# Kernel optimization log

Measured on AMD Instinct MI355X. Metric: run time of the kernel, lower is better.

Reference implementation:

```python
import jax, jax.numpy as jnp
import numpy as np

VOCAB, HID, EMB = 32000, 512, 256
N, L = 256, 512


def setup_inputs() -> dict:
    key = jax.random.key(0)
    ks = jax.random.split(key, 6)
    X = jax.random.randint(ks[0], (N, L), 0, VOCAB)
    emb = jax.random.normal(ks[1], (VOCAB, EMB), dtype=jnp.float32) * 0.02
    # torch Linear: y = x @ W.T + b, W shape (out, in)
    Whh_w = jax.random.normal(ks[2], (HID, HID), dtype=jnp.float32) * (1.0 / np.sqrt(HID))
    Whh_b = jnp.zeros((HID,), dtype=jnp.float32)
    Wxh_w = jax.random.normal(ks[3], (HID, EMB), dtype=jnp.float32) * (1.0 / np.sqrt(EMB))
    Wxh_b = jnp.zeros((HID,), dtype=jnp.float32)
    return {"X": X, "emb": emb, "Whh_w": Whh_w, "Whh_b": Whh_b,
            "Wxh_w": Wxh_w, "Wxh_b": Wxh_b}


def reference(X, emb, Whh_w, Whh_b, Wxh_w, Wxh_b):
    # X: (N, L) int ids -> last hidden state (N, H)
    E = emb[X]                       # (N, L, E) embedding lookup
    # precompute input projection for all timesteps (one big GEMM)
    XP = jnp.einsum('nle,he->nlh', E, Wxh_w) + Wxh_b  # (N, L, H)
    h0 = jnp.zeros((X.shape[0], Whh_w.shape[0]), dtype=emb.dtype)

    def step(h, xp_t):
        # xp_t: (N, H) at time t
        h_new = jnp.tanh(h @ Whh_w.T + Whh_b + xp_t)
        return h_new, None

    h_last, _ = jax.lax.scan(step, h0, jnp.swapaxes(XP, 0, 1))  # scan over L
    return h_last
```

## Files before the change

kernel.cpp:

```cpp
#include <hip/hip_runtime.h>
#include <hip/hip_bf16.h>
#include <math.h>

#define N_B    256
#define L_SEQ  512
#define HID    512
#define EMB_D  256

#define NGROUPS 16
#define GWGS    8

#define ESW_SHORTS_PER_BLK 8192
#define ESW_BYTES  ((size_t)NGROUPS * L_SEQ * ESW_SHORTS_PER_BLK * 2)
#define EX_UINTS_PER_SLOT (16 * HID)
#define EX_BYTES   ((size_t)2 * NGROUPS * EX_UINTS_PER_SLOT * 4)

typedef short v8s __attribute__((ext_vector_type(8)));
typedef float v4f __attribute__((ext_vector_type(4)));

static __device__ __forceinline__ unsigned short bf_bits(__hip_bfloat16 h) {
    union { __hip_bfloat16 b; unsigned short u; } c; c.b = h; return c.u;
}
static __device__ __forceinline__ void split_hilo(float v, short& hi, short& lo) {
    const __hip_bfloat16 h = __float2bfloat16(v);
    hi = (short)bf_bits(h);
    lo = (short)bf_bits(__float2bfloat16(v - __bfloat162float(h)));
}
static __device__ __forceinline__ void cvt8_hilo(const float* __restrict__ p,
                                                 v8s& hi, v8s& lo) {
    #pragma unroll
    for (int i = 0; i < 8; ++i) { short h, l; split_hilo(p[i], h, l); hi[i] = h; lo[i] = l; }
}
static __device__ __forceinline__ void gl_lds16(const short* g, short* l) {
    __builtin_amdgcn_global_load_lds(
        (const __attribute__((address_space(1))) unsigned int*)g,
        (__attribute__((address_space(3))) unsigned int*)l, 16, 0, 0);
}
static __device__ __forceinline__ float tanh_fast(float x) {
    const float z = __expf(2.0f * x);
    return 1.0f - 2.0f / (z + 1.0f);
}

__global__ __launch_bounds__(256) void esw_build(
    const int* __restrict__ X, const float* __restrict__ emb,
    short* __restrict__ Esw)
{
    const int bid = blockIdx.x;
    const int g = bid >> 9, t = bid & 511;
    short* base = Esw + (size_t)bid * ESW_SHORTS_PER_BLK;
    #pragma unroll
    for (int h = 0; h < 2; ++h) {
        const int f    = threadIdx.x + h * 256;
        const int kk   = f >> 6, lane = f & 63;
        const int m    = lane & 15, qp = lane >> 4;
        const int idx  = X[(g * 16 + m) * L_SEQ + t];
        const float* src = emb + (size_t)idx * EMB_D + kk * 32 + qp * 8;
        v8s hi8, lo8;
        cvt8_hilo(src, hi8, lo8);
        short* d = base + (size_t)(kk * 64 + lane) * 8;
        *(v8s*)d          = hi8;
        *(v8s*)(d + 4096) = lo8;
    }
}

__global__ __launch_bounds__(256, 1) void rnn_scan5(
    const float* __restrict__ Whh,
    const float* __restrict__ Whh_b,
    const float* __restrict__ Wxh,
    const float* __restrict__ Wxh_b,
    const short* __restrict__ Esw,
    unsigned int* __restrict__ ex,
    float* __restrict__ out)
{
    const int bid  = blockIdx.x;
    const int g    = bid & 15;
    const int j    = bid >> 4;
    const int tid  = threadIdx.x;
    const int w    = tid >> 6;
    const int l    = tid & 63;
    const int lo16 = l & 15;
    const int q    = l >> 4;
    const int cbase = j * 64 + w * 16;
    const int nbase = g * 16;

    __shared__ short ldsbuf[49152];
    __shared__ unsigned int tp[4][256];
    short* lds_h = ldsbuf;
    short* lds_e = ldsbuf + 32768;

    v8s bhi[16], blo[16];
    {
        const float* wp = Whh + (long)(cbase + lo16) * HID + q * 8;
        #pragma unroll
        for (int kk = 0; kk < 16; ++kk) cvt8_hilo(wp + kk * 32, bhi[kk], blo[kk]);
    }
    v8s xhi[8], xlo[8];
    {
        const float* wp = Wxh + (long)(cbase + lo16) * EMB_D + q * 8;
        #pragma unroll
        for (int kk = 0; kk < 8; ++kk) cvt8_hilo(wp + kk * 32, xhi[kk], xlo[kk]);
    }
    const int hcol = cbase + lo16;
    const float bias = Whh_b[hcol] + Wxh_b[hcol];

    const int region = (2 * j + (w >> 1)) * 512 + (w & 1) * 256;

    unsigned int* ex0 = ex + (size_t)g * EX_UINTS_PER_SLOT;
    unsigned int* ex1 = ex + (size_t)(NGROUPS + g) * EX_UINTS_PER_SLOT;
    const short* esrc = Esw + (size_t)(g * 512) * ESW_SHORTS_PER_BLK;

    #pragma unroll
    for (int c = 0; c < 4; ++c)
        gl_lds16(esrc + (w * 4 + c) * 512 + l * 8, lds_e + (w * 4 + c) * 512);
    __syncthreads();

    for (int t = 0; t < L_SEQ; ++t) {
        const int P = t & 1;
        short* lh = lds_h + P * 16384;
        short* le = lds_e + P * 8192;
        unsigned int* exsrc = P ? ex1 : ex0;
        unsigned int* exdst = P ? ex0 : ex1;

        if (t + 1 < L_SEQ) {
            const short* eb = esrc + (size_t)(t + 1) * ESW_SHORTS_PER_BLK;
            short* leN = lds_e + (P ^ 1) * 8192;
            #pragma unroll
            for (int c = 0; c < 4; ++c)
                gl_lds16(eb + (w * 4 + c) * 512 + l * 8, leN + (w * 4 + c) * 512);
        }

        v4f acc0 = {0,0,0,0}, acc1 = {0,0,0,0}, acc2 = {0,0,0,0};
        #pragma unroll
        for (int kk = 0; kk < 8; ++kk) {
            v8s ah = *(const v8s*)(le + (kk * 64 + l) * 8);
            v8s al = *(const v8s*)(le + 4096 + (kk * 64 + l) * 8);
            acc0 = __builtin_amdgcn_mfma_f32_16x16x32_bf16(ah, xhi[kk], acc0, 0, 0, 0);
            acc1 = __builtin_amdgcn_mfma_f32_16x16x32_bf16(ah, xlo[kk], acc1, 0, 0, 0);
            acc2 = __builtin_amdgcn_mfma_f32_16x16x32_bf16(al, xhi[kk], acc2, 0, 0, 0);
        }

        unsigned long long hv64[16];
        {
            const unsigned long long* hs = (const unsigned long long*)exsrc;
            const unsigned long long tagmask = 0x0001000000010000ull;
            const unsigned long long want = ((t >> 1) & 1) ? tagmask : 0ull;
            for (;;) {
                #pragma unroll
                for (int s = 0; s < 16; ++s)
                    hv64[s] = __hip_atomic_load(hs + s * 256 + tid,
                                                __ATOMIC_RELAXED,
                                                __HIP_MEMORY_SCOPE_AGENT);
                unsigned long long bad = 0;
                #pragma unroll
                for (int s = 0; s < 16; ++s) bad |= (hv64[s] ^ want) & tagmask;
                if (__all(bad == 0)) break;
            }
        }

        {
            unsigned int* lh_hi = (unsigned int*)lh;
            unsigned int* lh_lo = lh_hi + 4096;
            #pragma unroll
            for (int s = 0; s < 16; ++s) {
                const int o = s * 256 + tid;
                const unsigned int w0 = (unsigned int)hv64[s];
                const unsigned int w1 = (unsigned int)(hv64[s] >> 32);
                lh_hi[o] = (w0 & 0xffffu) | (w1 << 16);
                lh_lo[o] = (w0 >> 16)     | (w1 & 0xffff0000u);
            }
        }
        __syncthreads();

        #pragma unroll
        for (int kk = 0; kk < 16; ++kk) {
            v8s ah = *(const v8s*)(lh + (kk * 64 + l) * 8);
            v8s al = *(const v8s*)(lh + 8192 + (kk * 64 + l) * 8);
            acc0 = __builtin_amdgcn_mfma_f32_16x16x32_bf16(ah, bhi[kk], acc0, 0, 0, 0);
            acc1 = __builtin_amdgcn_mfma_f32_16x16x32_bf16(ah, blo[kk], acc1, 0, 0, 0);
            acc2 = __builtin_amdgcn_mfma_f32_16x16x32_bf16(al, bhi[kk], acc2, 0, 0, 0);
        }

        if (t < L_SEQ - 1) {
            const unsigned int wtag = (unsigned int)(((t + 1) >> 1) & 1) << 16;
            unsigned int* myt = tp[w];
            #pragma unroll
            for (int r = 0; r < 4; ++r) {
                const int m = q * 4 + r;
                const float pre = acc0[r] + acc1[r] + acc2[r] + bias;
                const float hv = tanh_fast(pre);
                short hi, lo; split_hilo(hv, hi, lo);
                unsigned int word = (unsigned int)(unsigned short)hi
                                  | ((unsigned int)(unsigned short)lo << 16);
                word = (word & 0xFFFEFFFFu) | wtag;
                myt[(m + 16 * (lo16 >> 3)) * 8 + (lo16 & 7)] = word;
            }
            asm volatile("s_waitcnt lgkmcnt(0)" ::: "memory");
            #pragma unroll
            for (int k = 0; k < 4; ++k) {
                const unsigned int val = myt[k * 64 + l];
                __hip_atomic_store(exdst + region + k * 64 + l, val,
                                   __ATOMIC_RELAXED, __HIP_MEMORY_SCOPE_AGENT);
            }
        } else {
            #pragma unroll
            for (int r = 0; r < 4; ++r) {
                const int m = q * 4 + r;
                const float pre = acc0[r] + acc1[r] + acc2[r] + bias;
                out[(long)(nbase + m) * HID + hcol] = tanh_fast(pre);
            }
        }
    }
}

extern "C" void kernel_launch(void* const* d_in, const int* in_sizes, int n_in,
                              void* d_out, int out_size, void* d_ws, size_t ws_size,
                              hipStream_t stream) {
    const int*   X     = (const int*)d_in[0];
    const float* emb   = (const float*)d_in[1];
    const float* Whh   = (const float*)d_in[2];
    const float* Whh_b = (const float*)d_in[3];
    const float* Wxh   = (const float*)d_in[4];
    const float* Wxh_b = (const float*)d_in[5];

    char* ws = (char*)d_ws;
    short*        Esw = (short*)ws;
    unsigned int* ex  = (unsigned int*)(ws + ESW_BYTES);

    hipMemsetAsync(ex, 0x00, EX_BYTES / 2, stream);
    hipMemsetAsync((char*)ex + EX_BYTES / 2, 0xFF, EX_BYTES / 2, stream);

    esw_build<<<dim3(NGROUPS * L_SEQ), dim3(256), 0, stream>>>(X, emb, Esw);
    rnn_scan5<<<dim3(NGROUPS * GWGS), dim3(256), 0, stream>>>(
        Whh, Whh_b, Wxh, Wxh_b, Esw, ex, (float*)d_out);
}
```

Measured before the change: 1.505 ms.

## Load hidden state directly into registers per wave, drop LDS staging and barrier

Each wave now polls and loads the full 512-wide hidden state from the global exchange buffer straight into registers in MFMA operand layout. This removes the LDS staging of h, the block-wide __syncthreads, and the cooperative split of polling across threads. The embedding operands are also read directly from global memory rather than prefetched into LDS with global_load_lds. In exchange, every wave loads 4x more data (64 u64 values per lane), which raises register pressure and global or L2 traffic on the critical serial path.

```diff
diff --git a/kernel.cpp b/kernel.cpp
--- a/kernel.cpp
+++ b/kernel.cpp
@@ -30,11 +30,6 @@
                                                  v8s& hi, v8s& lo) {
     #pragma unroll
     for (int i = 0; i < 8; ++i) { short h, l; split_hilo(p[i], h, l); hi[i] = h; lo[i] = l; }
-}
-static __device__ __forceinline__ void gl_lds16(const short* g, short* l) {
-    __builtin_amdgcn_global_load_lds(
-        (const __attribute__((address_space(1))) unsigned int*)g,
-        (__attribute__((address_space(3))) unsigned int*)l, 16, 0, 0);
 }
 static __device__ __forceinline__ float tanh_fast(float x) {
     const float z = __expf(2.0f * x);
@@ -63,7 +58,7 @@
     }
 }
 
-__global__ __launch_bounds__(256, 1) void rnn_scan5(
+__global__ __launch_bounds__(256, 1) void rnn_scan6(
     const float* __restrict__ Whh,
     const float* __restrict__ Whh_b,
     const float* __restrict__ Wxh,
@@ -83,10 +78,7 @@
     const int cbase = j * 64 + w * 16;
     const int nbase = g * 16;
 
-    __shared__ short ldsbuf[49152];
     __shared__ unsigned int tp[4][256];
-    short* lds_h = ldsbuf;
-    short* lds_e = ldsbuf + 32768;
 
     v8s bhi[16], blo[16];
     {
@@ -109,75 +101,66 @@
     unsigned int* ex1 = ex + (size_t)(NGROUPS + g) * EX_UINTS_PER_SLOT;
     const short* esrc = Esw + (size_t)(g * 512) * ESW_SHORTS_PER_BLK;
 
-    #pragma unroll
-    for (int c = 0; c < 4; ++c)
-        gl_lds16(esrc + (w * 4 + c) * 512 + l * 8, lds_e + (w * 4 + c) * 512);
-    __syncthreads();
-
     for (int t = 0; t < L_SEQ; ++t) {
         const int P = t & 1;
-        short* lh = lds_h + P * 16384;
-        short* le = lds_e + P * 8192;
-        unsigned int* exsrc = P ? ex1 : ex0;
+        const unsigned long long* exsrc =
+            (const unsigned long long*)(P ? ex1 : ex0);
         unsigned int* exdst = P ? ex0 : ex1;
 
-        if (t + 1 < L_SEQ) {
-            const short* eb = esrc + (size_t)(t + 1) * ESW_SHORTS_PER_BLK;
-            short* leN = lds_e + (P ^ 1) * 8192;
-            #pragma unroll
-            for (int c = 0; c < 4; ++c)
-                gl_lds16(eb + (w * 4 + c) * 512 + l * 8, leN + (w * 4 + c) * 512);
-        }
-
         v4f acc0 = {0,0,0,0}, acc1 = {0,0,0,0}, acc2 = {0,0,0,0};
-        #pragma unroll
-        for (int kk = 0; kk < 8; ++kk) {
-            v8s ah = *(const v8s*)(le + (kk * 64 + l) * 8);
-            v8s al = *(const v8s*)(le + 4096 + (kk * 64 + l) * 8);
-            acc0 = __builtin_amdgcn_mfma_f32_16x16x32_bf16(ah, xhi[kk], acc0, 0, 0, 0);
-            acc1 = __builtin_amdgcn_mfma_f32_16x16x32_bf16(ah, xlo[kk], acc1, 0, 0, 0);
-            acc2 = __builtin_amdgcn_mfma_f32_16x16x32_bf16(al, xhi[kk], acc2, 0, 0, 0);
-        }
-
-        unsigned long long hv64[16];
         {
-            const unsigned long long* hs = (const unsigned long long*)exsrc;
-            const unsigned long long tagmask = 0x0001000000010000ull;
-            const unsigned long long want = ((t >> 1) & 1) ? tagmask : 0ull;
-            for (;;) {
+            const short* eb = esrc + (size_t)t * ESW_SHORTS_PER_BLK;
+            #pragma unroll
+            for (int kk = 0; kk < 8; ++kk) {
+                v8s ah = *(const v8s*)(eb + (kk * 64 + l) * 8);
+                v8s al = *(const v8s*)(eb + 4096 + (kk * 64 + l) * 8);
+                acc0 = __builtin_amdgcn_mfma_f32_16x16x32_bf16(ah, xhi[kk], acc0, 0, 0, 0);
+                acc1 = __builtin_amdgcn_mfma_f32_16x16x32_bf16(ah, xlo[kk], acc1, 0, 0, 0);
+                acc2 = __builtin_amdgcn_mfma_f32_16x16x32_bf16(al, xhi[kk], acc2, 0, 0, 0);
+            }
+        }
+
+        unsigned long long hv[64];
+        {
+            const unsigned long long M = 0x0001000000010000ull;
+            const int want1 = (t >> 1) & 1;
+            bool pass;
+            do {
                 #pragma unroll
-                for (int s = 0; s < 16; ++s)
-                    hv64[s] = __hip_atomic_load(hs + s * 256 + tid,
-                                                __ATOMIC_RELAXED,
-                                                __HIP_MEMORY_SCOPE_AGENT);
-                unsigned long long bad = 0;
-                #pragma unroll
-                for (int s = 0; s < 16; ++s) bad |= (hv64[s] ^ want) & tagmask;
-                if (__all(bad == 0)) break;
-            }
-        }
-
-        {
-            unsigned int* lh_hi = (unsigned int*)lh;
-            unsigned int* lh_lo = lh_hi + 4096;
-            #pragma unroll
-            for (int s = 0; s < 16; ++s) {
-                const int o = s * 256 + tid;
-                const unsigned int w0 = (unsigned int)hv64[s];
-                const unsigned int w1 = (unsigned int)(hv64[s] >> 32);
-                lh_hi[o] = (w0 & 0xffffu) | (w1 << 16);
-                lh_lo[o] = (w0 >> 16)     | (w1 & 0xffff0000u);
-            }
-        }
-        __syncthreads();
+                for (int kk = 0; kk < 16; ++kk)
+                    #pragma unroll
+                    for (int ii = 0; ii < 4; ++ii)
+                        hv[kk * 4 + ii] = __hip_atomic_load(
+                            exsrc + kk * 256 + l * 4 + ii,
+                            __ATOMIC_RELAXED, __HIP_MEMORY_SCOPE_AGENT);
+                if (want1) {
+                    unsigned long long a = ~0ull;
+                    #pragma unroll
+                    for (int s = 0; s < 64; ++s) a &= hv[s];
+                    pass = ((a & M) == M);
+                } else {
+                    unsigned long long a = 0ull;
+                    #pragma unroll
+                    for (int s = 0; s < 64; ++s) a |= hv[s];
+                    pass = ((a & M) == 0ull);
+                }
+            } while (!__all(pass));
+        }
 
         #pragma unroll
         for (int kk = 0; kk < 16; ++kk) {
-            v8s ah = *(const v8s*)(lh + (kk * 64 + l) * 8);
-            v8s al = *(const v8s*)(lh + 8192 + (kk * 64 + l) * 8);
-            acc0 = __builtin_amdgcn_mfma_f32_16x16x32_bf16(ah, bhi[kk], acc0, 0, 0, 0);
-            acc1 = __builtin_amdgcn_mfma_f32_16x16x32_bf16(ah, blo[kk], acc1, 0, 0, 0);
-            acc2 = __builtin_amdgcn_mfma_f32_16x16x32_bf16(al, bhi[kk], acc2, 0, 0, 0);
+            union { v8s s; unsigned int u[4]; } ah, al;
+            #pragma unroll
+            for (int ii = 0; ii < 4; ++ii) {
+                const unsigned long long v = hv[kk * 4 + ii];
+                const unsigned int w0 = (unsigned int)v;
+                const unsigned int w1 = (unsigned int)(v >> 32);
+                ah.u[ii] = (w0 & 0xffffu) | (w1 << 16);
+                al.u[ii] = (w0 >> 16)     | (w1 & 0xffff0000u);
+            }
+            acc0 = __builtin_amdgcn_mfma_f32_16x16x32_bf16(ah.s, bhi[kk], acc0, 0, 0, 0);
+            acc1 = __builtin_amdgcn_mfma_f32_16x16x32_bf16(ah.s, blo[kk], acc1, 0, 0, 0);
+            acc2 = __builtin_amdgcn_mfma_f32_16x16x32_bf16(al.s, bhi[kk], acc2, 0, 0, 0);
         }
 
         if (t < L_SEQ - 1) {
@@ -187,8 +170,8 @@
             for (int r = 0; r < 4; ++r) {
                 const int m = q * 4 + r;
                 const float pre = acc0[r] + acc1[r] + acc2[r] + bias;
-                const float hv = tanh_fast(pre);
-                short hi, lo; split_hilo(hv, hi, lo);
+                const float hv2 = tanh_fast(pre);
+                short hi, lo; split_hilo(hv2, hi, lo);
                 unsigned int word = (unsigned int)(unsigned short)hi
                                   | ((unsigned int)(unsigned short)lo << 16);
                 word = (word & 0xFFFEFFFFu) | wtag;
@@ -230,6 +213,6 @@
     hipMemsetAsync((char*)ex + EX_BYTES / 2, 0xFF, EX_BYTES / 2, stream);
 
     esw_build<<<dim3(NGROUPS * L_SEQ), dim3(256), 0, stream>>>(X, emb, Esw);
-    rnn_scan5<<<dim3(NGROUPS * GWGS), dim3(256), 0, stream>>>(
+    rnn_scan6<<<dim3(NGROUPS * GWGS), dim3(256), 0, stream>>>(
         Whh, Whh_b, Wxh, Wxh_b, Esw, ex, (float*)d_out);
 }
```

After: 5.712 ms. 3.79x slower.
